# Performance work log

Hardware: AMD Instinct MI355X
Metric: run time of the kernel (lower is better)

Reference implementation:

```python
import jax, jax.numpy as jnp
import numpy as np

B, T, E, UNITS, VOCAB, NCLS = 128, 512, 256, 256, 50257, 2

def setup_inputs() -> dict:
    key = jax.random.key(0)
    ks = jax.random.split(key, 7)
    s = 0.05
    return {
        "sentence": jax.random.randint(ks[0], (B, T), 0, VOCAB, dtype=jnp.int32),
        "emb_table": jax.random.normal(ks[1], (VOCAB, E), jnp.float32) * s,
        "W": jax.random.normal(ks[2], (1, UNITS, E), jnp.float32) * s,
        "U": jax.random.normal(ks[3], (1, UNITS, UNITS), jnp.float32) * s,
        "W1": jax.random.normal(ks[4], (UNITS, 32), jnp.float32) * s,
        "b1": jnp.zeros((32,), jnp.float32),
        "W2": jax.random.normal(ks[5], (32, NCLS), jnp.float32) * s,
        "b2": jnp.zeros((NCLS,), jnp.float32),
    }

def reference(sentence, emb_table, W, U, W1, b1, W2, b2):
    # Embedding lookup: [B, T, E]
    emb = emb_table[sentence]
    # Precompute input projection for all timesteps in one batched GEMM:
    # x @ W[0].T for every t -> [T, B, units]
    xW = jnp.einsum('bte,ue->tbu', emb, W[0])
    Ut = U[0].T  # [units, units]

    def step(h, xw_t):
        h_new = jnp.tanh(xw_t + h @ Ut)
        return h_new, None

    h0 = jnp.zeros((sentence.shape[0], W.shape[1]), emb.dtype)
    h_final, _ = jax.lax.scan(step, h0, xW)

    # Classification head (dropout is identity at inference)
    hidden = jax.nn.relu(h_final @ W1 + b1)
    logits = hidden @ W2 + b2
    return jax.nn.softmax(logits, axis=-1)
```

## Files before the change

### kernel.cpp

```cpp
#include <hip/hip_runtime.h>
#include <hip/hip_bf16.h>
#include <stdint.h>

#define TT 512
#define NB 128
#define EM 256
#define UN 256

typedef float floatx4 __attribute__((ext_vector_type(4)));
typedef int v8i __attribute__((ext_vector_type(8)));

#define SCALE_Q 0x7B7B7B7BU
#define SCALE_A 0x7D7D7D7DU

#define BAR() asm volatile("s_waitcnt lgkmcnt(0)\n\ts_barrier" ::: "memory")

__device__ inline unsigned short f2bf(float f) {
    union { float f; uint32_t u; } v; v.f = f;
    uint32_t r = v.u + 0x7fffu + ((v.u >> 16) & 1u);
    return (unsigned short)(r >> 16);
}
__device__ inline unsigned char f2fp8(float f) {
    int pk = __builtin_amdgcn_cvt_pk_fp8_f32(f, f, 0, false);
    return (unsigned char)(pk & 0xff);
}
__device__ inline float fp8dec(uint32_t word, int sel) {
#if defined(__has_builtin)
#if __has_builtin(__builtin_amdgcn_cvt_f32_fp8)
    return __builtin_amdgcn_cvt_f32_fp8(word >> (8 * sel), 0);
#else
    unsigned char b = (word >> (8 * sel)) & 0xff;
    int s = b >> 7, e = (b >> 3) & 15, m = b & 7;
    float v = e ? ldexpf((float)(8 + m), e - 10) : ldexpf((float)m, -9);
    return s ? -v : v;
#endif
#else
    unsigned char b = (word >> (8 * sel)) & 0xff;
    int s = b >> 7, e = (b >> 3) & 15, m = b & 7;
    float v = e ? ldexpf((float)(8 + m), e - 10) : ldexpf((float)m, -9);
    return s ? -v : v;
#endif
}

__global__ void k_pack(const float* __restrict__ W, const float* __restrict__ U,
                       unsigned char* __restrict__ wfrag8, unsigned char* __restrict__ ufrag8) {
    int bid = blockIdx.x;
    const float* src = (bid < 32) ? W : U;
    unsigned char* dstbase = (bid < 32) ? wfrag8 : ufrag8;
    int idx = (bid & 31) * 256 + threadIdx.x;
    int jg   = idx & 3;
    int lane = (idx >> 2) & 63;
    int tile = idx >> 8;
    int nt = tile & 15, kh = tile >> 4;
    int u  = nt * 16 + (lane & 15);
    int k0 = kh * 128 + (lane >> 4) * 32 + jg * 8;
    unsigned char* dst = dstbase + ((size_t)tile * 64 + lane) * 32 + jg * 8;
    #pragma unroll
    for (int j = 0; j < 8; j++) dst[j] = f2fp8(16.f * src[u * EM + k0 + j]);
}

__global__ __launch_bounds__(256, 2) void k_gemm(
    const int* __restrict__ sent, const float* __restrict__ emb,
    const unsigned char* __restrict__ wfrag8, unsigned char* __restrict__ xw8)
{
    __shared__ unsigned char gt[64][272];
    int w    = threadIdx.x >> 6;
    int lane = threadIdx.x & 63;
    int m  = lane & 15;
    int kg = lane >> 4;
    int row = blockIdx.x * 64 + w * 16 + m;
    int tok = sent[row];
    const float* arow = emb + (size_t)tok * EM;

    union { uint32_t d[8]; v8i v; } A[2];
    #pragma unroll
    for (int kh = 0; kh < 2; kh++) {
        const float* p = arow + kh * 128 + kg * 32;
        #pragma unroll
        for (int d = 0; d < 8; d++) {
            float4 f = *(const float4*)(p + 4 * d);
            int pk = __builtin_amdgcn_cvt_pk_fp8_f32(16.f * f.x, 16.f * f.y, 0, false);
            pk     = __builtin_amdgcn_cvt_pk_fp8_f32(16.f * f.z, 16.f * f.w, pk, true);
            A[kh].d[d] = (uint32_t)pk;
        }
    }

    const floatx4 zero4 = {0.f, 0.f, 0.f, 0.f};
    floatx4 acc[16];
    #pragma unroll
    for (int nt = 0; nt < 16; nt++) {
        union { uint4 u4[2]; v8i v; } B0, B1;
        const uint4* p0 = (const uint4*)(wfrag8 + ((size_t)(0 * 16 + nt) * 64 + lane) * 32);
        const uint4* p1 = (const uint4*)(wfrag8 + ((size_t)(1 * 16 + nt) * 64 + lane) * 32);
        B0.u4[0] = p0[0]; B0.u4[1] = p0[1];
        B1.u4[0] = p1[0]; B1.u4[1] = p1[1];
        floatx4 a = __builtin_amdgcn_mfma_scale_f32_16x16x128_f8f6f4(
                        A[0].v, B0.v, zero4, 0, 0, 0, SCALE_Q, 0, SCALE_Q);
        a = __builtin_amdgcn_mfma_scale_f32_16x16x128_f8f6f4(
                        A[1].v, B1.v, a, 0, 0, 0, SCALE_Q, 0, SCALE_Q);
        acc[nt] = a;
    }

    int rloc = w * 16 + kg * 4;
    #pragma unroll
    for (int nt = 0; nt < 16; nt++) {
        #pragma unroll
        for (int r = 0; r < 4; r++) {
            gt[rloc + r][nt * 16 + m] = f2fp8(16.f * acc[nt][r]);
        }
    }
    __syncthreads();

    int rowbase = blockIdx.x * 64;
    #pragma unroll
    for (int r2 = 0; r2 < 16; r2++) {
        int rr = w * 16 + r2;
        uint32_t v = *(const uint32_t*)&gt[rr][lane * 4];
        *(uint32_t*)(xw8 + (size_t)(rowbase + rr) * UN + lane * 4) = v;
    }
}

__global__ __launch_bounds__(256, 1) void k_rnn(
    const unsigned char* __restrict__ ufrag8, const unsigned char* __restrict__ xw8,
    const float* __restrict__ W1, const float* __restrict__ b1,
    const float* __restrict__ W2, const float* __restrict__ b2,
    float* __restrict__ out)
{
    __shared__ __align__(16) unsigned char hb8[2][256];
    __shared__ __align__(16) unsigned char xstage[64 * 256];
    __shared__ float hid[32];
    const int t    = threadIdx.x;
    const int lane = t & 63;
    const int w    = t >> 6;
    const int kg   = lane >> 4;
    const int b    = blockIdx.x;

    v8i ufr8[4][2];
    #pragma unroll
    for (int q = 0; q < 4; q++) {
        #pragma unroll
        for (int kh = 0; kh < 2; kh++) {
            const uint4* p = (const uint4*)(ufrag8 + ((size_t)(kh * 16 + 4 * w + q) * 64 + lane) * 32);
            union { uint4 u4[2]; v8i v; } cvt;
            cvt.u4[0] = p[0]; cvt.u4[1] = p[1];
            ufr8[q][kh] = cvt.v;
        }
    }

    const unsigned char* xwb = xw8 + (size_t)b * TT * UN;
    const int roff = t * 16;

    uint4 xr[4];
    #pragma unroll
    for (int p = 0; p < 4; p++) xr[p] = *(const uint4*)(xwb + roff + p * 4096);
    #pragma unroll
    for (int p = 0; p < 4; p++) *(uint4*)&xstage[roff + p * 4096] = xr[p];

    hb8[0][t] = 0; hb8[1][t] = 0;
    __syncthreads();

    int cur = 0;
    const float c3 = -0.33333334f, c5 = 0.13333334f, c7 = -0.05396825f, c9 = 0.02186949f;
    const floatx4 zero4 = {0.f, 0.f, 0.f, 0.f};
    const int sel = lane >> 4;

    for (int s = 0; s < TT; s++) {
        const int ls = s & 63;
        uint32_t xword = *(const uint32_t*)&xstage[ls * 256 + (t & ~3)];
        float xf = fp8dec(xword, t & 3) * 0.0625f;

        const unsigned char* hc = hb8[cur];
        union { uint4 u4[2]; v8i v; } A0, A1;
        A0.u4[0] = *(const uint4*)(hc + kg * 32);
        A0.u4[1] = *(const uint4*)(hc + kg * 32 + 16);
        A1.u4[0] = *(const uint4*)(hc + 128 + kg * 32);
        A1.u4[1] = *(const uint4*)(hc + 128 + kg * 32 + 16);

        float z[4];
        #pragma unroll
        for (int q = 0; q < 4; q++) {
            floatx4 acc = __builtin_amdgcn_mfma_scale_f32_16x16x128_f8f6f4(
                              A0.v, ufr8[q][0], zero4, 0, 0, 0, SCALE_A, 0, SCALE_Q);
            acc = __builtin_amdgcn_mfma_scale_f32_16x16x128_f8f6f4(
                              A1.v, ufr8[q][1], acc, 0, 0, 0, SCALE_A, 0, SCALE_Q);
            z[q] = acc[0];
        }

        float zz = (sel == 0) ? z[0] : (sel == 1) ? z[1] : (sel == 2) ? z[2] : z[3];
        zz += xf;

        float hn;
        if (__builtin_expect(fabsf(zz) > 0.75f, 0)) {
            float e = __expf(2.f * zz);
            hn = 1.f - 2.f * __builtin_amdgcn_rcpf(e + 1.f);
        } else {
            float x2f = zz * zz;
            float p = fmaf(x2f, c9, c7);
            p = fmaf(x2f, p, c5);
            p = fmaf(x2f, p, c3);
            hn = fmaf(zz * x2f, p, zz);
        }

        hb8[cur ^ 1][t] = f2fp8(4.f * hn);

        if (ls == 60 && s + 68 <= TT) {
            const unsigned char* cb = xwb + (size_t)(s + 4) * UN;
            #pragma unroll
            for (int p = 0; p < 4; p++) xr[p] = *(const uint4*)(cb + roff + p * 4096);
        }
        if (ls == 63 && s + 65 <= TT) {
            BAR();
            #pragma unroll
            for (int p = 0; p < 4; p++) *(uint4*)&xstage[roff + p * 4096] = xr[p];
        }
        BAR();
        cur ^= 1;
    }

    if (t < 32) {
        float a = b1[t];
        for (int k = 0; k < 256; k++) {
            uint32_t wd = *(const uint32_t*)&hb8[cur][k & ~3];
            a += 0.25f * fp8dec(wd, k & 3) * W1[k * 32 + t];
        }
        hid[t] = fmaxf(a, 0.f);
    }
    __syncthreads();
    if (t == 0) {
        float l0 = b2[0], l1 = b2[1];
        #pragma unroll
        for (int i = 0; i < 32; i++) {
            float hv = hid[i];
            l0 += hv * W2[2 * i];
            l1 += hv * W2[2 * i + 1];
        }
        float mx2 = fmaxf(l0, l1);
        float e0 = __expf(l0 - mx2), e1 = __expf(l1 - mx2);
        float inv = 1.f / (e0 + e1);
        out[2 * b]     = e0 * inv;
        out[2 * b + 1] = e1 * inv;
    }
}

extern "C" void kernel_launch(void* const* d_in, const int* in_sizes, int n_in,
                              void* d_out, int out_size, void* d_ws, size_t ws_size,
                              hipStream_t stream) {
    const int*   sent = (const int*)d_in[0];
    const float* emb  = (const float*)d_in[1];
    const float* W    = (const float*)d_in[2];
    const float* U    = (const float*)d_in[3];
    const float* W1   = (const float*)d_in[4];
    const float* b1   = (const float*)d_in[5];
    const float* W2   = (const float*)d_in[6];
    const float* b2   = (const float*)d_in[7];
    float* out = (float*)d_out;

    unsigned char* xw8    = (unsigned char*)d_ws;
    unsigned char* wfrag8 = (unsigned char*)d_ws + (size_t)NB * TT * UN;
    unsigned char* ufrag8 = wfrag8 + (size_t)UN * EM;

    k_pack<<<64, 256, 0, stream>>>(W, U, wfrag8, ufrag8);
    k_gemm<<<(NB * TT) / 64, 256, 0, stream>>>(sent, emb, wfrag8, xw8);
    k_rnn<<<NB, 256, 0, stream>>>(ufrag8, xw8, W1, b1, W2, b2, out);
}
```

Measured before the change: 304.3 us.

## Fuse input-projection GEMM into RNN kernel with double-buffered per-chunk bursts

Removes the separate k_gemm launch and its global round-trip of the fp8 xW buffer. Each RNN block now computes the input projection for its next 64 timesteps in an MFMA burst, writing into a second LDS stage buffer with an XOR swizzle. The embedding gather is spread across earlier steps of the loop. This adds work and register pressure inside the serial recurrence, which is the critical path, and only 128 blocks do the GEMM.

After: 308.1 us. No clear change (+1.2%).

```diff
diff --git a/kernel.cpp b/kernel.cpp
--- a/kernel.cpp
+++ b/kernel.cpp
@@ -1,5 +1,4 @@
 #include <hip/hip_runtime.h>
-#include <hip/hip_bf16.h>
 #include <stdint.h>
 
 #define TT 512
@@ -15,11 +14,6 @@
 
 #define BAR() asm volatile("s_waitcnt lgkmcnt(0)\n\ts_barrier" ::: "memory")
 
-__device__ inline unsigned short f2bf(float f) {
-    union { float f; uint32_t u; } v; v.f = f;
-    uint32_t r = v.u + 0x7fffu + ((v.u >> 16) & 1u);
-    return (unsigned short)(r >> 16);
-}
 __device__ inline unsigned char f2fp8(float f) {
     int pk = __builtin_amdgcn_cvt_pk_fp8_f32(f, f, 0, false);
     return (unsigned char)(pk & 0xff);
@@ -59,80 +53,57 @@
     for (int j = 0; j < 8; j++) dst[j] = f2fp8(16.f * src[u * EM + k0 + j]);
 }
 
-__global__ __launch_bounds__(256, 2) void k_gemm(
-    const int* __restrict__ sent, const float* __restrict__ emb,
-    const unsigned char* __restrict__ wfrag8, unsigned char* __restrict__ xw8)
+__device__ inline void gemm_burst(const unsigned char* __restrict__ wfrag8,
+                                  const float4* araw, unsigned char* dst,
+                                  int w, int m, int kg, int lane)
 {
-    __shared__ unsigned char gt[64][272];
-    int w    = threadIdx.x >> 6;
-    int lane = threadIdx.x & 63;
-    int m  = lane & 15;
-    int kg = lane >> 4;
-    int row = blockIdx.x * 64 + w * 16 + m;
-    int tok = sent[row];
-    const float* arow = emb + (size_t)tok * EM;
-
-    union { uint32_t d[8]; v8i v; } A[2];
+    union { uint32_t d[8]; v8i v; } B[2];
     #pragma unroll
     for (int kh = 0; kh < 2; kh++) {
-        const float* p = arow + kh * 128 + kg * 32;
-        #pragma unroll
-        for (int d = 0; d < 8; d++) {
-            float4 f = *(const float4*)(p + 4 * d);
+        #pragma unroll
+        for (int d2 = 0; d2 < 8; d2++) {
+            float4 f = araw[kh * 8 + d2];
             int pk = __builtin_amdgcn_cvt_pk_fp8_f32(16.f * f.x, 16.f * f.y, 0, false);
             pk     = __builtin_amdgcn_cvt_pk_fp8_f32(16.f * f.z, 16.f * f.w, pk, true);
-            A[kh].d[d] = (uint32_t)pk;
-        }
-    }
-
+            B[kh].d[d2] = (uint32_t)pk;
+        }
+    }
     const floatx4 zero4 = {0.f, 0.f, 0.f, 0.f};
-    floatx4 acc[16];
-    #pragma unroll
-    for (int nt = 0; nt < 16; nt++) {
-        union { uint4 u4[2]; v8i v; } B0, B1;
-        const uint4* p0 = (const uint4*)(wfrag8 + ((size_t)(0 * 16 + nt) * 64 + lane) * 32);
-        const uint4* p1 = (const uint4*)(wfrag8 + ((size_t)(1 * 16 + nt) * 64 + lane) * 32);
-        B0.u4[0] = p0[0]; B0.u4[1] = p0[1];
-        B1.u4[0] = p1[0]; B1.u4[1] = p1[1];
-        floatx4 a = __builtin_amdgcn_mfma_scale_f32_16x16x128_f8f6f4(
-                        A[0].v, B0.v, zero4, 0, 0, 0, SCALE_Q, 0, SCALE_Q);
-        a = __builtin_amdgcn_mfma_scale_f32_16x16x128_f8f6f4(
-                        A[1].v, B1.v, a, 0, 0, 0, SCALE_Q, 0, SCALE_Q);
-        acc[nt] = a;
-    }
-
-    int rloc = w * 16 + kg * 4;
-    #pragma unroll
-    for (int nt = 0; nt < 16; nt++) {
-        #pragma unroll
-        for (int r = 0; r < 4; r++) {
-            gt[rloc + r][nt * 16 + m] = f2fp8(16.f * acc[nt][r]);
-        }
-    }
-    __syncthreads();
-
-    int rowbase = blockIdx.x * 64;
-    #pragma unroll
-    for (int r2 = 0; r2 < 16; r2++) {
-        int rr = w * 16 + r2;
-        uint32_t v = *(const uint32_t*)&gt[rr][lane * 4];
-        *(uint32_t*)(xw8 + (size_t)(rowbase + rr) * UN + lane * 4) = v;
+    const int lsout = w * 16 + m;
+    const int sw = (lsout & 7) << 3;
+    #pragma unroll
+    for (int ut = 0; ut < 16; ut++) {
+        union { uint4 u4[2]; v8i v; } A0, A1;
+        const uint4* p0 = (const uint4*)(wfrag8 + ((size_t)(ut)      * 64 + lane) * 32);
+        const uint4* p1 = (const uint4*)(wfrag8 + ((size_t)(16 + ut) * 64 + lane) * 32);
+        A0.u4[0] = p0[0]; A0.u4[1] = p0[1];
+        A1.u4[0] = p1[0]; A1.u4[1] = p1[1];
+        floatx4 acc = __builtin_amdgcn_mfma_scale_f32_16x16x128_f8f6f4(
+                          A0.v, B[0].v, zero4, 0, 0, 0, SCALE_Q, 0, SCALE_Q);
+        acc = __builtin_amdgcn_mfma_scale_f32_16x16x128_f8f6f4(
+                          A1.v, B[1].v, acc, 0, 0, 0, SCALE_Q, 0, SCALE_Q);
+        int pk = __builtin_amdgcn_cvt_pk_fp8_f32(16.f * acc[0], 16.f * acc[1], 0, false);
+        pk     = __builtin_amdgcn_cvt_pk_fp8_f32(16.f * acc[2], 16.f * acc[3], pk, true);
+        int wi = (ut * 4 + kg) ^ sw;
+        *(uint32_t*)(dst + (size_t)lsout * 256 + wi * 4) = (uint32_t)pk;
     }
 }
 
 __global__ __launch_bounds__(256, 1) void k_rnn(
-    const unsigned char* __restrict__ ufrag8, const unsigned char* __restrict__ xw8,
+    const int* __restrict__ sent, const float* __restrict__ emb,
+    const unsigned char* __restrict__ wfrag8, const unsigned char* __restrict__ ufrag8,
     const float* __restrict__ W1, const float* __restrict__ b1,
     const float* __restrict__ W2, const float* __restrict__ b2,
     float* __restrict__ out)
 {
     __shared__ __align__(16) unsigned char hb8[2][256];
-    __shared__ __align__(16) unsigned char xstage[64 * 256];
+    __shared__ __align__(16) unsigned char xstage[2][64 * 256];
     __shared__ float hid[32];
     const int t    = threadIdx.x;
     const int lane = t & 63;
     const int w    = t >> 6;
     const int kg   = lane >> 4;
+    const int m    = lane & 15;
     const int b    = blockIdx.x;
 
     v8i ufr8[4][2];
@@ -147,29 +118,33 @@
         }
     }
 
-    const unsigned char* xwb = xw8 + (size_t)b * TT * UN;
-    const int roff = t * 16;
-
-    uint4 xr[4];
-    #pragma unroll
-    for (int p = 0; p < 4; p++) xr[p] = *(const uint4*)(xwb + roff + p * 4096);
-    #pragma unroll
-    for (int p = 0; p < 4; p++) *(uint4*)&xstage[roff + p * 4096] = xr[p];
+    float4 araw[16];
+    int tok = sent[b * TT + w * 16 + m];
+    {
+        const float* arow = emb + (size_t)tok * EM + kg * 32;
+        #pragma unroll
+        for (int kh = 0; kh < 2; kh++)
+            #pragma unroll
+            for (int d = 0; d < 8; d++)
+                araw[kh * 8 + d] = *(const float4*)(arow + kh * 128 + 4 * d);
+    }
+    gemm_burst(wfrag8, araw, &xstage[0][0], w, m, kg, lane);
 
     hb8[0][t] = 0; hb8[1][t] = 0;
     __syncthreads();
 
-    int cur = 0;
+    int hcur = 0, xcur = 0;
     const float c3 = -0.33333334f, c5 = 0.13333334f, c7 = -0.05396825f, c9 = 0.02186949f;
     const floatx4 zero4 = {0.f, 0.f, 0.f, 0.f};
     const int sel = lane >> 4;
 
     for (int s = 0; s < TT; s++) {
         const int ls = s & 63;
-        uint32_t xword = *(const uint32_t*)&xstage[ls * 256 + (t & ~3)];
+        int wi = (t >> 2) ^ ((ls & 7) << 3);
+        uint32_t xword = *(const uint32_t*)&xstage[xcur][ls * 256 + wi * 4];
         float xf = fp8dec(xword, t & 3) * 0.0625f;
 
-        const unsigned char* hc = hb8[cur];
+        const unsigned char* hc = hb8[hcur];
         union { uint4 u4[2]; v8i v; } A0, A1;
         A0.u4[0] = *(const uint4*)(hc + kg * 32);
         A0.u4[1] = *(const uint4*)(hc + kg * 32 + 16);
@@ -201,26 +176,34 @@
             hn = fmaf(zz * x2f, p, zz);
         }
 
-        hb8[cur ^ 1][t] = f2fp8(4.f * hn);
-
-        if (ls == 60 && s + 68 <= TT) {
-            const unsigned char* cb = xwb + (size_t)(s + 4) * UN;
-            #pragma unroll
-            for (int p = 0; p < 4; p++) xr[p] = *(const uint4*)(cb + roff + p * 4096);
-        }
-        if (ls == 63 && s + 65 <= TT) {
-            BAR();
-            #pragma unroll
-            for (int p = 0; p < 4; p++) *(uint4*)&xstage[roff + p * 4096] = xr[p];
-        }
+        hb8[hcur ^ 1][t] = f2fp8(4.f * hn);
+
+        int nbase = (s & ~63) + 64;
+        if (nbase < TT) {
+            if (ls == 12) {
+                tok = sent[b * TT + nbase + w * 16 + m];
+            }
+            if (ls == 16) {
+                const float* arow = emb + (size_t)tok * EM + kg * 32;
+                #pragma unroll
+                for (int kh = 0; kh < 2; kh++)
+                    #pragma unroll
+                    for (int d = 0; d < 8; d++)
+                        araw[kh * 8 + d] = *(const float4*)(arow + kh * 128 + 4 * d);
+            }
+            if (ls == 24) {
+                gemm_burst(wfrag8, araw, &xstage[xcur ^ 1][0], w, m, kg, lane);
+            }
+        }
+        if (ls == 63) xcur ^= 1;
         BAR();
-        cur ^= 1;
+        hcur ^= 1;
     }
 
     if (t < 32) {
         float a = b1[t];
         for (int k = 0; k < 256; k++) {
-            uint32_t wd = *(const uint32_t*)&hb8[cur][k & ~3];
+            uint32_t wd = *(const uint32_t*)&hb8[hcur][k & ~3];
             a += 0.25f * fp8dec(wd, k & 3) * W1[k * 32 + t];
         }
         hid[t] = fmaxf(a, 0.f);
@@ -255,11 +238,9 @@
     const float* b2   = (const float*)d_in[7];
     float* out = (float*)d_out;
 
-    unsigned char* xw8    = (unsigned char*)d_ws;
-    unsigned char* wfrag8 = (unsigned char*)d_ws + (size_t)NB * TT * UN;
+    unsigned char* wfrag8 = (unsigned char*)d_ws;
     unsigned char* ufrag8 = wfrag8 + (size_t)UN * EM;
 
     k_pack<<<64, 256, 0, stream>>>(W, U, wfrag8, ufrag8);
-    k_gemm<<<(NB * TT) / 64, 256, 0, stream>>>(sent, emb, wfrag8, xw8);
-    k_rnn<<<NB, 256, 0, stream>>>(ufrag8, xw8, W1, b1, W2, b2, out);
-}
+    k_rnn<<<NB, 256, 0, stream>>>(sent, emb, wfrag8, ufrag8, W1, b1, W2, b2, out);
+}
```

## Unroll RNN step loop with static ping-pong buffers and split MFMA chains

Applied to the files above, without the earlier changes.

Restructures the recurrent loop into a chunked, manually unrolled loop where the h ping-pong buffers are two separate static arrays with precomputed pointers, removing per-step index arithmetic and the conditional prefetch checks. It splits each dependent pair of MFMAs into two independent accumulators summed afterwards, shortening the serial MFMA dependency chain on the critical per-step path. The classifier head's first layer is parallelised across all 256 threads with a partial-sum reduction instead of 32 threads looping over 256 inputs. The trade-offs are higher register pressure and larger code size.

New measurement: 346.7 us. +13.9%, slower.

```diff
diff --git a/kernel.cpp b/kernel.cpp
--- a/kernel.cpp
+++ b/kernel.cpp
@@ -1,5 +1,4 @@
 #include <hip/hip_runtime.h>
-#include <hip/hip_bf16.h>
 #include <stdint.h>
 
 #define TT 512
@@ -15,11 +14,6 @@
 
 #define BAR() asm volatile("s_waitcnt lgkmcnt(0)\n\ts_barrier" ::: "memory")
 
-__device__ inline unsigned short f2bf(float f) {
-    union { float f; uint32_t u; } v; v.f = f;
-    uint32_t r = v.u + 0x7fffu + ((v.u >> 16) & 1u);
-    return (unsigned short)(r >> 16);
-}
 __device__ inline unsigned char f2fp8(float f) {
     int pk = __builtin_amdgcn_cvt_pk_fp8_f32(f, f, 0, false);
     return (unsigned char)(pk & 0xff);
@@ -126,8 +120,10 @@
     const float* __restrict__ W2, const float* __restrict__ b2,
     float* __restrict__ out)
 {
-    __shared__ __align__(16) unsigned char hb8[2][256];
+    __shared__ __align__(16) unsigned char hb0[256];
+    __shared__ __align__(16) unsigned char hb1[256];
     __shared__ __align__(16) unsigned char xstage[64 * 256];
+    __shared__ float partial[256];
     __shared__ float hid[32];
     const int t    = threadIdx.x;
     const int lane = t & 63;
@@ -156,37 +152,49 @@
     #pragma unroll
     for (int p = 0; p < 4; p++) *(uint4*)&xstage[roff + p * 4096] = xr[p];
 
-    hb8[0][t] = 0; hb8[1][t] = 0;
-    __syncthreads();
-
-    int cur = 0;
+    hb0[t] = 0; hb1[t] = 0;
+    __syncthreads();
+
     const float c3 = -0.33333334f, c5 = 0.13333334f, c7 = -0.05396825f, c9 = 0.02186949f;
     const floatx4 zero4 = {0.f, 0.f, 0.f, 0.f};
-    const int sel = lane >> 4;
-
-    for (int s = 0; s < TT; s++) {
-        const int ls = s & 63;
-        uint32_t xword = *(const uint32_t*)&xstage[ls * 256 + (t & ~3)];
+    const int sel = kg;
+    const unsigned char* h0a = hb0 + kg * 32;
+    const unsigned char* h0b = hb0 + 128 + kg * 32;
+    const unsigned char* h1a = hb1 + kg * 32;
+    const unsigned char* h1b = hb1 + 128 + kg * 32;
+    const unsigned char* xsl = xstage + (t & ~3);
+
+    auto STEP = [&](int ls, const unsigned char* ha, const unsigned char* hb2,
+                    unsigned char* hdst) {
+        uint32_t xword = *(const uint32_t*)(xsl + ls * 256);
         float xf = fp8dec(xword, t & 3) * 0.0625f;
 
-        const unsigned char* hc = hb8[cur];
         union { uint4 u4[2]; v8i v; } A0, A1;
-        A0.u4[0] = *(const uint4*)(hc + kg * 32);
-        A0.u4[1] = *(const uint4*)(hc + kg * 32 + 16);
-        A1.u4[0] = *(const uint4*)(hc + 128 + kg * 32);
-        A1.u4[1] = *(const uint4*)(hc + 128 + kg * 32 + 16);
-
-        float z[4];
-        #pragma unroll
-        for (int q = 0; q < 4; q++) {
-            floatx4 acc = __builtin_amdgcn_mfma_scale_f32_16x16x128_f8f6f4(
-                              A0.v, ufr8[q][0], zero4, 0, 0, 0, SCALE_A, 0, SCALE_Q);
-            acc = __builtin_amdgcn_mfma_scale_f32_16x16x128_f8f6f4(
-                              A1.v, ufr8[q][1], acc, 0, 0, 0, SCALE_A, 0, SCALE_Q);
-            z[q] = acc[0];
-        }
-
-        float zz = (sel == 0) ? z[0] : (sel == 1) ? z[1] : (sel == 2) ? z[2] : z[3];
+        A0.u4[0] = *(const uint4*)ha;        A0.u4[1] = *(const uint4*)(ha + 16);
+        A1.u4[0] = *(const uint4*)hb2;       A1.u4[1] = *(const uint4*)(hb2 + 16);
+
+        floatx4 a00 = __builtin_amdgcn_mfma_scale_f32_16x16x128_f8f6f4(
+                          A0.v, ufr8[0][0], zero4, 0, 0, 0, SCALE_A, 0, SCALE_Q);
+        floatx4 a01 = __builtin_amdgcn_mfma_scale_f32_16x16x128_f8f6f4(
+                          A1.v, ufr8[0][1], zero4, 0, 0, 0, SCALE_A, 0, SCALE_Q);
+        floatx4 a10 = __builtin_amdgcn_mfma_scale_f32_16x16x128_f8f6f4(
+                          A0.v, ufr8[1][0], zero4, 0, 0, 0, SCALE_A, 0, SCALE_Q);
+        floatx4 a11 = __builtin_amdgcn_mfma_scale_f32_16x16x128_f8f6f4(
+                          A1.v, ufr8[1][1], zero4, 0, 0, 0, SCALE_A, 0, SCALE_Q);
+        floatx4 a20 = __builtin_amdgcn_mfma_scale_f32_16x16x128_f8f6f4(
+                          A0.v, ufr8[2][0], zero4, 0, 0, 0, SCALE_A, 0, SCALE_Q);
+        floatx4 a21 = __builtin_amdgcn_mfma_scale_f32_16x16x128_f8f6f4(
+                          A1.v, ufr8[2][1], zero4, 0, 0, 0, SCALE_A, 0, SCALE_Q);
+        floatx4 a30 = __builtin_amdgcn_mfma_scale_f32_16x16x128_f8f6f4(
+                          A0.v, ufr8[3][0], zero4, 0, 0, 0, SCALE_A, 0, SCALE_Q);
+        floatx4 a31 = __builtin_amdgcn_mfma_scale_f32_16x16x128_f8f6f4(
+                          A1.v, ufr8[3][1], zero4, 0, 0, 0, SCALE_A, 0, SCALE_Q);
+        float z0 = a00[0] + a01[0];
+        float z1 = a10[0] + a11[0];
+        float z2 = a20[0] + a21[0];
+        float z3 = a30[0] + a31[0];
+
+        float zz = (sel == 0) ? z0 : (sel == 1) ? z1 : (sel == 2) ? z2 : z3;
         zz += xf;
 
         float hn;
@@ -200,30 +208,48 @@
             p = fmaf(x2f, p, c3);
             hn = fmaf(zz * x2f, p, zz);
         }
-
-        hb8[cur ^ 1][t] = f2fp8(4.f * hn);
-
-        if (ls == 60 && s + 68 <= TT) {
-            const unsigned char* cb = xwb + (size_t)(s + 4) * UN;
+        hdst[t] = f2fp8(4.f * hn);
+    };
+
+    for (int c = 0; c < 8; ++c) {
+        for (int i = 0; i < 30; ++i) {
+            STEP(2 * i,     h0a, h0b, hb1); BAR();
+            STEP(2 * i + 1, h1a, h1b, hb0); BAR();
+        }
+        STEP(60, h0a, h0b, hb1);
+        if (c < 7) {
+            const unsigned char* cb = xwb + (size_t)(c + 1) * 64 * 256;
             #pragma unroll
             for (int p = 0; p < 4; p++) xr[p] = *(const uint4*)(cb + roff + p * 4096);
         }
-        if (ls == 63 && s + 65 <= TT) {
-            BAR();
+        BAR();
+        STEP(61, h1a, h1b, hb0); BAR();
+        STEP(62, h0a, h0b, hb1); BAR();
+        STEP(63, h1a, h1b, hb0); BAR();
+        if (c < 7) {
             #pragma unroll
             for (int p = 0; p < 4; p++) *(uint4*)&xstage[roff + p * 4096] = xr[p];
         }
         BAR();
-        cur ^= 1;
-    }
-
+    }
+
+    {
+        int col = t & 31, seg = t >> 5;
+        float a = 0.f;
+        #pragma unroll
+        for (int kk = 0; kk < 32; kk++) {
+            int k = seg * 32 + kk;
+            uint32_t wd = *(const uint32_t*)&hb0[k & ~3];
+            a += fp8dec(wd, k & 3) * W1[k * 32 + col];
+        }
+        partial[t] = a;
+    }
+    __syncthreads();
     if (t < 32) {
-        float a = b1[t];
-        for (int k = 0; k < 256; k++) {
-            uint32_t wd = *(const uint32_t*)&hb8[cur][k & ~3];
-            a += 0.25f * fp8dec(wd, k & 3) * W1[k * 32 + t];
-        }
-        hid[t] = fmaxf(a, 0.f);
+        float acc = 0.f;
+        #pragma unroll
+        for (int i = 0; i < 8; i++) acc += partial[i * 32 + t];
+        hid[t] = fmaxf(fmaf(0.25f, acc, b1[t]), 0.f);
     }
     __syncthreads();
     if (t == 0) {
```
